# Optimization experiments

Hardware: AMD Instinct MI355X
Metric: run time of the kernel (lower is better)

The kernel has to match this reference:

```python
import jax, jax.numpy as jnp
import numpy as np

HIDDEN = 2048
N_HEADS = 16
N_KV = 4
HEAD_DIM = HIDDEN // N_HEADS  # 128


def setup_inputs() -> dict:
    key = jax.random.key(0)
    ks = jax.random.split(key, 9)
    s = 0.02
    kv_dim = N_KV * HEAD_DIM
    return {
        "x": jax.random.normal(ks[0], (2, 2048, HIDDEN), dtype=jnp.float32),
        "wq": jax.random.normal(ks[1], (HIDDEN, HIDDEN), dtype=jnp.float32) * s,
        "bq": jnp.zeros((HIDDEN,), jnp.float32),
        "wk": jax.random.normal(ks[2], (HIDDEN, kv_dim), dtype=jnp.float32) * s,
        "bk": jnp.zeros((kv_dim,), jnp.float32),
        "wv": jax.random.normal(ks[3], (HIDDEN, kv_dim), dtype=jnp.float32) * s,
        "bv": jnp.zeros((kv_dim,), jnp.float32),
        "wo": jax.random.normal(ks[4], (HIDDEN, HIDDEN), dtype=jnp.float32) * s,
        "bo": jnpp if False else jnp.zeros((HIDDEN,), jnp.float32),
    }


def reference(x, wq, bq, wk, bk, wv, bv, wo, bo):
    b, s, _ = x.shape
    rep = N_HEADS // N_KV
    # projections -> [b, heads, s, d]
    q = (x @ wq + bq).reshape(b, s, N_HEADS, HEAD_DIM).transpose(0, 2, 1, 3)
    k = (x @ wk + bk).reshape(b, s, N_KV, HEAD_DIM).transpose(0, 2, 1, 3)
    v = (x @ wv + bv).reshape(b, s, N_KV, HEAD_DIM).transpose(0, 2, 1, 3)
    # repeat_interleave KV heads to match Q heads
    k = jnp.repeat(k, rep, axis=1)
    v = jnp.repeat(v, rep, axis=1)
    scores = jnp.einsum("bhqd,bhkd->bhqk", q, k) / jnp.sqrt(jnp.float32(HEAD_DIM))
    attn = jax.nn.softmax(scores, axis=-1)  # dropout: eval mode (identity)
    out = jnp.einsum("bhqk,bhkd->bhqd", attn, v)
    out = out.transpose(0, 2, 1, 3).reshape(b, s, HIDDEN)
    return out @ wo + bo
```

## Files before the change

kernel.cpp:

```cpp
#include <hip/hip_runtime.h>

typedef short bf16x8 __attribute__((ext_vector_type(8)));
typedef float f32x4 __attribute__((ext_vector_type(4)));

__device__ __forceinline__ unsigned short f2b(float f) {
  union { float f; unsigned int u; } c; c.f = f;
  unsigned int u = c.u + 0x7fffu + ((c.u >> 16) & 1u);
  return (unsigned short)(u >> 16);
}

__device__ __forceinline__ void ld_g2l16(const void* g, void* l) {
  __builtin_amdgcn_global_load_lds(
      (__attribute__((address_space(1))) void*)(void*)g,
      (__attribute__((address_space(3))) void*)l, 16, 0, 0);
}


__global__ __launch_bounds__(256) void k_cvt(const float* __restrict__ in,
                                             unsigned short* __restrict__ out, int n) {
  int i = (blockIdx.x * 256 + threadIdx.x) * 4;
  const int stride = gridDim.x * 256 * 4;
  for (; i < n; i += stride) {
    const float4 v = *(const float4*)(in + i);
    unsigned short o0 = f2b(v.x), o1 = f2b(v.y), o2 = f2b(v.z), o3 = f2b(v.w);
    ushort4 o; o.x = o0; o.y = o1; o.z = o2; o.w = o3;
    *(ushort4*)(out + i) = o;
  }
}

__global__ __launch_bounds__(256) void k_tw(const float* __restrict__ W,
                                            unsigned short* __restrict__ Wt, int K, int N) {
  __shared__ float tile[32][33];
  const int nb = blockIdx.x * 32, kb = blockIdx.y * 32;
  const int tx = threadIdx.x & 31, ty = threadIdx.x >> 5;
#pragma unroll
  for (int i = 0; i < 32; i += 8)
    tile[ty + i][tx] = W[(size_t)(kb + ty + i) * N + nb + tx];
  __syncthreads();
#pragma unroll
  for (int i = 0; i < 32; i += 8)
    Wt[(size_t)(nb + ty + i) * K + kb + tx] = f2b(tile[tx][ty + i]);
}

__global__ __launch_bounds__(256) void k_tv(const unsigned short* __restrict__ v,
                                            unsigned short* __restrict__ vT) {
  __shared__ unsigned short tile[32][33];
  const int sb = blockIdx.x * 32, db = blockIdx.y * 32;
  const int ob = blockIdx.z, b = ob >> 2, kvh = ob & 3;
  const int tx = threadIdx.x & 31, ty = threadIdx.x >> 5;
#pragma unroll
  for (int i = 0; i < 32; i += 8)
    tile[ty + i][tx] = v[(size_t)(b * 2048 + sb + ty + i) * 1024 + 512 + kvh * 128 + db + tx];
  __syncthreads();
#pragma unroll
  for (int i = 0; i < 32; i += 8)
    vT[(size_t)ob * 262144 + (size_t)(db + ty + i) * 2048 + sb + tx] = tile[tx][ty + i];
}


template <int OUT_F32>
__global__ __launch_bounds__(256) void gemm_bt(const unsigned short* __restrict__ A,
                                               const unsigned short* __restrict__ Bt,
                                               const float* __restrict__ bias,
                                               const float* __restrict__ bias2,
                                               int nsplit,
                                               void* __restrict__ Cout,
                                               int M, int N, int K) {
  __shared__ unsigned short As[8192] __attribute__((aligned(16)));
  __shared__ unsigned short Bs[8192] __attribute__((aligned(16)));
  const int t = threadIdx.x, w = t >> 6, lane = t & 63;
  const int wr = w >> 1, wc = w & 1;
  const int bm = blockIdx.y, bn = blockIdx.x;

  f32x4 acc[4][4] = {};

  const int srow = w * 8 + (lane >> 3);
  const int scol = ((lane & 7) ^ (lane >> 3)) << 3;
  const unsigned short* Ap = A + (size_t)(bm * 128 + srow) * K + scol;
  const unsigned short* Bp = Bt + (size_t)(bn * 128 + srow) * K + scol;
  unsigned short* Ad = &As[(w * 64 + lane) * 8];
  unsigned short* Bd = &Bs[(w * 64 + lane) * 8];

  const int nkt = K >> 6;
  for (int kt = 0; kt < nkt; ++kt) {
#pragma unroll
    for (int i = 0; i < 4; ++i) {
      ld_g2l16(Ap + (size_t)i * 32 * K, Ad + i * 2048);
      ld_g2l16(Bp + (size_t)i * 32 * K, Bd + i * 2048);
    }
    Ap += 64; Bp += 64;
    __syncthreads();
#pragma unroll
    for (int kk = 0; kk < 2; ++kk) {
      bf16x8 av[4], bv[4];
#pragma unroll
      for (int m = 0; m < 4; ++m) {
        int r = wr * 64 + m * 16 + (lane & 15);
        int c = ((kk << 2) + (lane >> 4)) ^ (r & 7);
        av[m] = *(const bf16x8*)&As[r * 64 + c * 8];
      }
#pragma unroll
      for (int n = 0; n < 4; ++n) {
        int r = wc * 64 + n * 16 + (lane & 15);
        int c = ((kk << 2) + (lane >> 4)) ^ (r & 7);
        bv[n] = *(const bf16x8*)&Bs[r * 64 + c * 8];
      }
#pragma unroll
      for (int m = 0; m < 4; ++m)
#pragma unroll
        for (int n = 0; n < 4; ++n)
          acc[m][n] = __builtin_amdgcn_mfma_f32_16x16x32_bf16(av[m], bv[n], acc[m][n], 0, 0, 0);
    }
    __syncthreads();
  }

  const int row0 = bm * 128 + wr * 64 + ((lane >> 4) << 2);
  const int col0 = bn * 128 + wc * 64 + (lane & 15);
#pragma unroll
  for (int n = 0; n < 4; ++n) {
    const int c = col0 + n * 16;
    const float bb = (c < nsplit) ? bias[c] : bias2[c - nsplit];
#pragma unroll
    for (int m = 0; m < 4; ++m) {
#pragma unroll
      for (int j = 0; j < 4; ++j) {
        const float v = acc[m][n][j] + bb;
        const size_t idx = (size_t)(row0 + m * 16 + j) * N + c;
        if (OUT_F32) ((float*)Cout)[idx] = v;
        else ((unsigned short*)Cout)[idx] = f2b(v);
      }
    }
  }
}


__global__ __launch_bounds__(256, 4) void flash_gqa(const unsigned short* __restrict__ Q,
                                                    const unsigned short* __restrict__ Kx,
                                                    const unsigned short* __restrict__ Vt,
                                                    unsigned short* __restrict__ Oa) {
  __shared__ unsigned short smem[20480] __attribute__((aligned(16)));
  unsigned short* const Qs = smem;
  unsigned short* const Ks = smem;
  unsigned short* const Vs = smem + 8192;
  unsigned short* const Ps = smem + 16384;

  const int t = threadIdx.x, w = t >> 6, lane = t & 63;
  const int qt = blockIdx.x, bh = blockIdx.y;
  const int b = bh >> 4, h = bh & 15, kvh = h >> 2;

  const unsigned short* Qg = Q + (size_t)(b * 2048 + qt * 64) * 2048 + h * 128;
  const unsigned short* Kg = Kx + (size_t)(b * 2048) * 1024 + kvh * 128;
  const unsigned short* Vg = Vt + (size_t)(b * 4 + kvh) * 262144;

  {
    const int sc = ((t & 15) ^ ((t >> 4) & 7)) << 3;
    const unsigned short* src = Qg + (size_t)(t >> 4) * 2048 + sc;
    unsigned short* dst = &Qs[t * 8];
#pragma unroll
    for (int i = 0; i < 4; ++i) ld_g2l16(src + (size_t)i * 16 * 2048, dst + i * 2048);
  }
  __syncthreads();
  bf16x8 qf[4];
  {
    const int qr = w * 16 + (lane & 15);
#pragma unroll
    for (int kk = 0; kk < 4; ++kk) {
      const int c = ((kk << 2) + (lane >> 4)) ^ (qr & 7);
      qf[kk] = *(const bf16x8*)&Qs[qr * 128 + c * 8];
    }
  }
  __syncthreads();

  const float SC2 = 0.1275174246f;
  float m_run[4], l_run[4];
#pragma unroll
  for (int j = 0; j < 4; ++j) { m_run[j] = -1e30f; l_run[j] = 0.f; }
  f32x4 oacc[8] = {};

  const int ksc = ((t & 15) ^ ((t >> 4) & 7)) << 3;
  const int vsc = ((t & 7) ^ ((t >> 3) & 7)) << 3;
  unsigned short* const Kd = &Ks[t * 8];
  unsigned short* const Vd = &Vs[t * 8];

  for (int kt = 0; kt < 32; ++kt) {
    const unsigned short* ks = Kg + (size_t)(kt * 64 + (t >> 4)) * 1024 + ksc;
    const unsigned short* vs = Vg + (size_t)(t >> 3) * 2048 + kt * 64 + vsc;
#pragma unroll
    for (int i = 0; i < 4; ++i) {
      ld_g2l16(ks + (size_t)i * 16 * 1024, Kd + i * 2048);
      ld_g2l16(vs + (size_t)i * 32 * 2048, Vd + i * 2048);
    }
    __syncthreads();

    f32x4 sac[4] = {};
#pragma unroll
    for (int kk = 0; kk < 4; ++kk) {
      bf16x8 kf[4];
#pragma unroll
      for (int n = 0; n < 4; ++n) {
        const int r = n * 16 + (lane & 15);
        const int c = ((kk << 2) + (lane >> 4)) ^ (r & 7);
        kf[n] = *(const bf16x8*)&Ks[r * 128 + c * 8];
      }
#pragma unroll
      for (int n = 0; n < 4; ++n)
        sac[n] = __builtin_amdgcn_mfma_f32_16x16x32_bf16(qf[kk], kf[n], sac[n], 0, 0, 0);
    }

#pragma unroll
    for (int n = 0; n < 4; ++n)
#pragma unroll
      for (int j = 0; j < 4; ++j) sac[n][j] *= SC2;
#pragma unroll
    for (int j = 0; j < 4; ++j) {
      float tm = fmaxf(fmaxf(sac[0][j], sac[1][j]), fmaxf(sac[2][j], sac[3][j]));
#pragma unroll
      for (int off = 1; off < 16; off <<= 1) tm = fmaxf(tm, __shfl_xor(tm, off, 64));
      const float mn = fmaxf(m_run[j], tm);
      const float corr = exp2f(m_run[j] - mn);
      m_run[j] = mn;
      float rs = 0.f;
#pragma unroll
      for (int n = 0; n < 4; ++n) {
        const float p = exp2f(sac[n][j] - mn);
        sac[n][j] = p;
        rs += p;
      }
#pragma unroll
      for (int off = 1; off < 16; off <<= 1) rs += __shfl_xor(rs, off, 64);
      l_run[j] = l_run[j] * corr + rs;
#pragma unroll
      for (int di = 0; di < 8; ++di) oacc[di][j] *= corr;
    }

    {
      const int rbase = w * 16 + ((lane >> 4) << 2);
#pragma unroll
      for (int j = 0; j < 4; ++j) {
        const int r = rbase + j;
#pragma unroll
        for (int n = 0; n < 4; ++n) {
          const int col = n * 16 + (lane & 15);
          Ps[r * 64 + (((col >> 3) ^ (r & 7)) << 3) + (lane & 7)] = f2b(sac[n][j]);
        }
      }
    }

#pragma unroll
    for (int kk = 0; kk < 2; ++kk) {
      const int pr = w * 16 + (lane & 15);
      const int pc = ((kk << 2) + (lane >> 4)) ^ (pr & 7);
      const bf16x8 pf = *(const bf16x8*)&Ps[pr * 64 + pc * 8];
#pragma unroll
      for (int di = 0; di < 8; ++di) {
        const int r = di * 16 + (lane & 15);
        const int c = ((kk << 2) + (lane >> 4)) ^ (r & 7);
        const bf16x8 vf = *(const bf16x8*)&Vs[r * 64 + c * 8];
        oacc[di] = __builtin_amdgcn_mfma_f32_16x16x32_bf16(pf, vf, oacc[di], 0, 0, 0);
      }
    }
    __syncthreads();
  }

  {
    const int rbase = b * 2048 + qt * 64 + w * 16 + ((lane >> 4) << 2);
#pragma unroll
    for (int j = 0; j < 4; ++j) {
      const float inv = 1.0f / l_run[j];
#pragma unroll
      for (int di = 0; di < 8; ++di) {
        const int col = h * 128 + di * 16 + (lane & 15);
        Oa[(size_t)(rbase + j) * 2048 + col] = f2b(oacc[di][j] * inv);
      }
    }
  }
}


extern "C" void kernel_launch(void* const* d_in, const int* in_sizes, int n_in,
                              void* d_out, int out_size, void* d_ws, size_t ws_size,
                              hipStream_t stream) {
  (void)in_sizes; (void)n_in; (void)out_size; (void)ws_size;
  const float* x  = (const float*)d_in[0];
  const float* wq = (const float*)d_in[1];
  const float* bq = (const float*)d_in[2];
  const float* wk = (const float*)d_in[3];
  const float* bk = (const float*)d_in[4];
  const float* wv = (const float*)d_in[5];
  const float* bv = (const float*)d_in[6];
  const float* wo = (const float*)d_in[7];
  const float* bo = (const float*)d_in[8];

  char* ws = (char*)d_ws;
  unsigned short* xb  = (unsigned short*)(ws);
  unsigned short* qb  = (unsigned short*)(ws + 16777216);
  unsigned short* kvb = (unsigned short*)(ws + 33554432);
  unsigned short* vT  = (unsigned short*)(ws + 41943040);
  unsigned short* wqT = (unsigned short*)(ws + 46137344);
  unsigned short* wkT = (unsigned short*)(ws + 54525952);
  unsigned short* woT = (unsigned short*)(ws + 58720256);
  unsigned short* wvT = (unsigned short*)(ws + 56623104);

  k_cvt<<<4096, 256, 0, stream>>>(x, xb, 4096 * 2048);
  k_tw<<<dim3(64, 64), 256, 0, stream>>>(wq, wqT, 2048, 2048);
  k_tw<<<dim3(16, 64), 256, 0, stream>>>(wk, wkT, 2048, 512);
  k_tw<<<dim3(16, 64), 256, 0, stream>>>(wv, wvT, 2048, 512);
  k_tw<<<dim3(64, 64), 256, 0, stream>>>(wo, woT, 2048, 2048);

  gemm_bt<0><<<dim3(16, 32), 256, 0, stream>>>(xb, wqT, bq, bq, 1 << 30, qb, 4096, 2048, 2048);
  gemm_bt<0><<<dim3(8, 32), 256, 0, stream>>>(xb, wkT, bk, bv, 512, kvb, 4096, 1024, 2048);

  k_tv<<<dim3(64, 4, 8), 256, 0, stream>>>(kvb, vT);

  unsigned short* ao = xb;
  flash_gqa<<<dim3(32, 32), 256, 0, stream>>>(qb, kvb, vT, ao);

  gemm_bt<1><<<dim3(16, 32), 256, 0, stream>>>(ao, woT, bo, bo, 1 << 30, (float*)d_out, 4096, 2048, 2048);
}
```

Baseline: 425.8 us.

## Rewrite flash attention with 32x32 MFMA, transposed S, double-buffered K/V

The attention kernel now processes 128 query rows per block, with each wave owning 32 rows, and uses 32x32x16 MFMAs computing S^T so that P stays in registers (cvt_pk plus permlane32 swap) instead of going through shared memory. K/V tiles are double-buffered so the next tile's global-to-LDS load overlaps with compute. The online softmax rescale is skipped unless the max grows by more than a threshold, and the output is staged through LDS for coalesced 16-byte stores. This adds register pressure and doubles LDS use (occupancy hint drops to 2) and halves the grid.

```diff
diff --git a/kernel.cpp b/kernel.cpp
--- a/kernel.cpp
+++ b/kernel.cpp
@@ -2,11 +2,23 @@
 
 typedef short bf16x8 __attribute__((ext_vector_type(8)));
 typedef float f32x4 __attribute__((ext_vector_type(4)));
+typedef float f32x16 __attribute__((ext_vector_type(16)));
+typedef unsigned int u32;
 
 __device__ __forceinline__ unsigned short f2b(float f) {
   union { float f; unsigned int u; } c; c.f = f;
   unsigned int u = c.u + 0x7fffu + ((c.u >> 16) & 1u);
   return (unsigned short)(u >> 16);
+}
+
+__device__ __forceinline__ u32 cvtpk(float a, float b) {
+  u32 r;
+  asm("v_cvt_pk_bf16_f32 %0, %1, %2" : "=v"(r) : "v"(a), "v"(b));
+  return r;
+}
+
+__device__ __forceinline__ void pswap(u32& a, u32& b) {
+  asm("v_permlane32_swap_b32 %0, %1" : "+v"(a), "+v"(b));
 }
 
 __device__ __forceinline__ void ld_g2l16(const void* g, void* l) {
@@ -134,144 +146,185 @@
 }
 
 
-__global__ __launch_bounds__(256, 4) void flash_gqa(const unsigned short* __restrict__ Q,
+__global__ __launch_bounds__(256, 2) void flash_gqa(const unsigned short* __restrict__ Q,
                                                     const unsigned short* __restrict__ Kx,
                                                     const unsigned short* __restrict__ Vt,
                                                     unsigned short* __restrict__ Oa) {
-  __shared__ unsigned short smem[20480] __attribute__((aligned(16)));
-  unsigned short* const Qs = smem;
-  unsigned short* const Ks = smem;
-  unsigned short* const Vs = smem + 8192;
-  unsigned short* const Ps = smem + 16384;
-
+  __shared__ unsigned short smem[32768] __attribute__((aligned(16)));
   const int t = threadIdx.x, w = t >> 6, lane = t & 63;
+  const int lo = lane & 31, hi1 = lane >> 5;
   const int qt = blockIdx.x, bh = blockIdx.y;
   const int b = bh >> 4, h = bh & 15, kvh = h >> 2;
 
-  const unsigned short* Qg = Q + (size_t)(b * 2048 + qt * 64) * 2048 + h * 128;
+  const unsigned short* Qg = Q + (size_t)(b * 2048 + qt * 128) * 2048 + h * 128;
   const unsigned short* Kg = Kx + (size_t)(b * 2048) * 1024 + kvh * 128;
   const unsigned short* Vg = Vt + (size_t)(b * 4 + kvh) * 262144;
 
   {
     const int sc = ((t & 15) ^ ((t >> 4) & 7)) << 3;
     const unsigned short* src = Qg + (size_t)(t >> 4) * 2048 + sc;
-    unsigned short* dst = &Qs[t * 8];
-#pragma unroll
-    for (int i = 0; i < 4; ++i) ld_g2l16(src + (size_t)i * 16 * 2048, dst + i * 2048);
-  }
-  __syncthreads();
-  bf16x8 qf[4];
+    unsigned short* dst = &smem[t * 8];
+#pragma unroll
+    for (int i = 0; i < 8; ++i) ld_g2l16(src + (size_t)i * 16 * 2048, dst + i * 2048);
+  }
+  __syncthreads();
+  bf16x8 qf[8];
   {
-    const int qr = w * 16 + (lane & 15);
-#pragma unroll
-    for (int kk = 0; kk < 4; ++kk) {
-      const int c = ((kk << 2) + (lane >> 4)) ^ (qr & 7);
-      qf[kk] = *(const bf16x8*)&Qs[qr * 128 + c * 8];
-    }
-  }
-  __syncthreads();
+    const int r = w * 32 + lo;
+#pragma unroll
+    for (int kk = 0; kk < 8; ++kk) {
+      const int c8 = (2 * kk + hi1) ^ (r & 7);
+      qf[kk] = *(const bf16x8*)&smem[r * 128 + c8 * 8];
+    }
+  }
+  __syncthreads();
+
+  unsigned short* const K0 = smem;
+  unsigned short* const V0 = smem + 8192;
+  unsigned short* const K1 = smem + 16384;
+  unsigned short* const V1 = smem + 24576;
+
+  const int kchunk_src = ((t & 15) ^ ((t >> 4) & 7)) << 3;
+  const int vchunk_src = ((t & 7) ^ ((t >> 3) & 7)) << 3;
+
+  auto stage = [&](int kt, unsigned short* Kd, unsigned short* Vd) {
+    const unsigned short* ks = Kg + (size_t)(kt * 64 + (t >> 4)) * 1024 + kchunk_src;
+    const unsigned short* vs = Vg + (size_t)(t >> 3) * 2048 + kt * 64 + vchunk_src;
+#pragma unroll
+    for (int i = 0; i < 4; ++i) {
+      ld_g2l16(ks + (size_t)i * 16384, Kd + t * 8 + i * 2048);
+      ld_g2l16(vs + (size_t)i * 65536, Vd + t * 8 + i * 2048);
+    }
+  };
 
   const float SC2 = 0.1275174246f;
-  float m_run[4], l_run[4];
-#pragma unroll
-  for (int j = 0; j < 4; ++j) { m_run[j] = -1e30f; l_run[j] = 0.f; }
-  f32x4 oacc[8] = {};
-
-  const int ksc = ((t & 15) ^ ((t >> 4) & 7)) << 3;
-  const int vsc = ((t & 7) ^ ((t >> 3) & 7)) << 3;
-  unsigned short* const Kd = &Ks[t * 8];
-  unsigned short* const Vd = &Vs[t * 8];
+  float m_run = -1e30f, l_run = 0.f;
+  f32x16 oT[4] = {};
+
+  stage(0, K0, V0);
+  __syncthreads();
 
   for (int kt = 0; kt < 32; ++kt) {
-    const unsigned short* ks = Kg + (size_t)(kt * 64 + (t >> 4)) * 1024 + ksc;
-    const unsigned short* vs = Vg + (size_t)(t >> 3) * 2048 + kt * 64 + vsc;
+    unsigned short* const Kc = (kt & 1) ? K1 : K0;
+    unsigned short* const Vc = (kt & 1) ? V1 : V0;
+    if (kt < 31) stage(kt + 1, (kt & 1) ? K0 : K1, (kt & 1) ? V0 : V1);
+
+    f32x16 sa0 = {}, sa1 = {};
+    __builtin_amdgcn_s_setprio(1);
+#pragma unroll
+    for (int kk = 0; kk < 8; ++kk) {
+      const int c8 = (2 * kk + hi1) ^ (lo & 7);
+      const bf16x8 kf0 = *(const bf16x8*)&Kc[lo * 128 + c8 * 8];
+      const bf16x8 kf1 = *(const bf16x8*)&Kc[(32 + lo) * 128 + c8 * 8];
+      sa0 = __builtin_amdgcn_mfma_f32_32x32x16_bf16(kf0, qf[kk], sa0, 0, 0, 0);
+      sa1 = __builtin_amdgcn_mfma_f32_32x32x16_bf16(kf1, qf[kk], sa1, 0, 0, 0);
+    }
+    __builtin_amdgcn_s_setprio(0);
+
+    float tmax[8];
+#pragma unroll
+    for (int i = 0; i < 8; ++i) tmax[i] = fmaxf(sa0[i], sa0[i + 8]);
+#pragma unroll
+    for (int i = 0; i < 8; ++i) tmax[i] = fmaxf(tmax[i], fmaxf(sa1[i], sa1[i + 8]));
+    float tm = fmaxf(fmaxf(fmaxf(tmax[0], tmax[1]), fmaxf(tmax[2], tmax[3])),
+                     fmaxf(fmaxf(tmax[4], tmax[5]), fmaxf(tmax[6], tmax[7])));
+    tm *= SC2;
+    tm = fmaxf(tm, __shfl_xor(tm, 32, 64));
+
+    if (!__all(tm <= m_run + 8.f)) {
+      const float mn = fmaxf(m_run, tm);
+      const float corr = exp2f(m_run - mn);
+      m_run = mn;
+      l_run *= corr;
+#pragma unroll
+      for (int d = 0; d < 4; ++d)
+#pragma unroll
+        for (int i = 0; i < 16; ++i) oT[d][i] *= corr;
+    }
+
+    float r0 = 0.f, r1 = 0.f, r2 = 0.f, r3 = 0.f;
 #pragma unroll
     for (int i = 0; i < 4; ++i) {
-      ld_g2l16(ks + (size_t)i * 16 * 1024, Kd + i * 2048);
-      ld_g2l16(vs + (size_t)i * 32 * 2048, Vd + i * 2048);
-    }
+      float p0 = exp2f(fmaf(sa0[i], SC2, -m_run));      sa0[i] = p0;      r0 += p0;
+      float p1 = exp2f(fmaf(sa0[i + 4], SC2, -m_run));  sa0[i + 4] = p1;  r1 += p1;
+      float p2 = exp2f(fmaf(sa0[i + 8], SC2, -m_run));  sa0[i + 8] = p2;  r2 += p2;
+      float p3 = exp2f(fmaf(sa0[i + 12], SC2, -m_run)); sa0[i + 12] = p3; r3 += p3;
+    }
+#pragma unroll
+    for (int i = 0; i < 4; ++i) {
+      float p0 = exp2f(fmaf(sa1[i], SC2, -m_run));      sa1[i] = p0;      r0 += p0;
+      float p1 = exp2f(fmaf(sa1[i + 4], SC2, -m_run));  sa1[i + 4] = p1;  r1 += p1;
+      float p2 = exp2f(fmaf(sa1[i + 8], SC2, -m_run));  sa1[i + 8] = p2;  r2 += p2;
+      float p3 = exp2f(fmaf(sa1[i + 12], SC2, -m_run)); sa1[i + 12] = p3; r3 += p3;
+    }
+    float rs = (r0 + r1) + (r2 + r3);
+    rs += __shfl_xor(rs, 32, 64);
+    l_run += rs;
+
+    bf16x8 pf[4];
+#pragma unroll
+    for (int m = 0; m < 4; ++m) {
+      const int base = (m & 1) * 8;
+      u32 alo, ahi, blo, bhi;
+      if (m < 2) {
+        alo = cvtpk(sa0[base + 0], sa0[base + 1]);
+        ahi = cvtpk(sa0[base + 2], sa0[base + 3]);
+        blo = cvtpk(sa0[base + 4], sa0[base + 5]);
+        bhi = cvtpk(sa0[base + 6], sa0[base + 7]);
+      } else {
+        alo = cvtpk(sa1[base + 0], sa1[base + 1]);
+        ahi = cvtpk(sa1[base + 2], sa1[base + 3]);
+        blo = cvtpk(sa1[base + 4], sa1[base + 5]);
+        bhi = cvtpk(sa1[base + 6], sa1[base + 7]);
+      }
+      pswap(alo, blo);
+      pswap(ahi, bhi);
+      union { u32 u[4]; bf16x8 v; } pk;
+      pk.u[0] = alo; pk.u[1] = ahi; pk.u[2] = blo; pk.u[3] = bhi;
+      pf[m] = pk.v;
+    }
+
+    __builtin_amdgcn_s_setprio(1);
+#pragma unroll
+    for (int m = 0; m < 4; ++m) {
+#pragma unroll
+      for (int d = 0; d < 4; ++d) {
+        const int r = d * 32 + lo;
+        const int c = (2 * m + hi1) ^ (lo & 7);
+        const bf16x8 vf = *(const bf16x8*)&Vc[r * 64 + c * 8];
+        oT[d] = __builtin_amdgcn_mfma_f32_32x32x16_bf16(vf, pf[m], oT[d], 0, 0, 0);
+      }
+    }
+    __builtin_amdgcn_s_setprio(0);
     __syncthreads();
-
-    f32x4 sac[4] = {};
-#pragma unroll
-    for (int kk = 0; kk < 4; ++kk) {
-      bf16x8 kf[4];
-#pragma unroll
-      for (int n = 0; n < 4; ++n) {
-        const int r = n * 16 + (lane & 15);
-        const int c = ((kk << 2) + (lane >> 4)) ^ (r & 7);
-        kf[n] = *(const bf16x8*)&Ks[r * 128 + c * 8];
-      }
-#pragma unroll
-      for (int n = 0; n < 4; ++n)
-        sac[n] = __builtin_amdgcn_mfma_f32_16x16x32_bf16(qf[kk], kf[n], sac[n], 0, 0, 0);
-    }
-
-#pragma unroll
-    for (int n = 0; n < 4; ++n)
-#pragma unroll
-      for (int j = 0; j < 4; ++j) sac[n][j] *= SC2;
-#pragma unroll
-    for (int j = 0; j < 4; ++j) {
-      float tm = fmaxf(fmaxf(sac[0][j], sac[1][j]), fmaxf(sac[2][j], sac[3][j]));
-#pragma unroll
-      for (int off = 1; off < 16; off <<= 1) tm = fmaxf(tm, __shfl_xor(tm, off, 64));
-      const float mn = fmaxf(m_run[j], tm);
-      const float corr = exp2f(m_run[j] - mn);
-      m_run[j] = mn;
-      float rs = 0.f;
-#pragma unroll
-      for (int n = 0; n < 4; ++n) {
-        const float p = exp2f(sac[n][j] - mn);
-        sac[n][j] = p;
-        rs += p;
-      }
-#pragma unroll
-      for (int off = 1; off < 16; off <<= 1) rs += __shfl_xor(rs, off, 64);
-      l_run[j] = l_run[j] * corr + rs;
-#pragma unroll
-      for (int di = 0; di < 8; ++di) oacc[di][j] *= corr;
-    }
-
-    {
-      const int rbase = w * 16 + ((lane >> 4) << 2);
-#pragma unroll
-      for (int j = 0; j < 4; ++j) {
-        const int r = rbase + j;
-#pragma unroll
-        for (int n = 0; n < 4; ++n) {
-          const int col = n * 16 + (lane & 15);
-          Ps[r * 64 + (((col >> 3) ^ (r & 7)) << 3) + (lane & 7)] = f2b(sac[n][j]);
+  }
+
+  const float inv = 1.0f / l_run;
+  u32* const Ot = (u32*)smem;
+  {
+    const int row = w * 32 + lo;
+#pragma unroll
+    for (int d = 0; d < 4; ++d) {
+#pragma unroll
+      for (int j2 = 0; j2 < 4; ++j2) {
+#pragma unroll
+        for (int p = 0; p < 2; ++p) {
+          const int rg = 4 * j2 + 2 * p;
+          const u32 pk = cvtpk(oT[d][rg] * inv, oT[d][rg + 1] * inv);
+          const int dw = d * 16 + 4 * j2 + 2 * hi1 + p;
+          Ot[row * 64 + (((dw >> 2) ^ (row & 15)) << 2) + (dw & 3)] = pk;
         }
       }
     }
-
-#pragma unroll
-    for (int kk = 0; kk < 2; ++kk) {
-      const int pr = w * 16 + (lane & 15);
-      const int pc = ((kk << 2) + (lane >> 4)) ^ (pr & 7);
-      const bf16x8 pf = *(const bf16x8*)&Ps[pr * 64 + pc * 8];
-#pragma unroll
-      for (int di = 0; di < 8; ++di) {
-        const int r = di * 16 + (lane & 15);
-        const int c = ((kk << 2) + (lane >> 4)) ^ (r & 7);
-        const bf16x8 vf = *(const bf16x8*)&Vs[r * 64 + c * 8];
-        oacc[di] = __builtin_amdgcn_mfma_f32_16x16x32_bf16(pf, vf, oacc[di], 0, 0, 0);
-      }
-    }
-    __syncthreads();
-  }
-
+  }
+  __syncthreads();
   {
-    const int rbase = b * 2048 + qt * 64 + w * 16 + ((lane >> 4) << 2);
-#pragma unroll
-    for (int j = 0; j < 4; ++j) {
-      const float inv = 1.0f / l_run[j];
-#pragma unroll
-      for (int di = 0; di < 8; ++di) {
-        const int col = h * 128 + di * 16 + (lane & 15);
-        Oa[(size_t)(rbase + j) * 2048 + col] = f2b(oacc[di][j] * inv);
-      }
+#pragma unroll
+    for (int i = 0; i < 8; ++i) {
+      const int row = i * 16 + (t >> 4);
+      const int c4 = (t & 15) ^ (row & 15);
+      const int4 val = *(const int4*)&Ot[row * 64 + c4 * 4];
+      *(int4*)&Oa[(size_t)(b * 2048 + qt * 128 + row) * 2048 + h * 128 + (t & 15) * 8] = val;
     }
   }
 }
@@ -298,8 +351,8 @@
   unsigned short* vT  = (unsigned short*)(ws + 41943040);
   unsigned short* wqT = (unsigned short*)(ws + 46137344);
   unsigned short* wkT = (unsigned short*)(ws + 54525952);
+  unsigned short* wvT = (unsigned short*)(ws + 56623104);
   unsigned short* woT = (unsigned short*)(ws + 58720256);
-  unsigned short* wvT = (unsigned short*)(ws + 56623104);
 
   k_cvt<<<4096, 256, 0, stream>>>(x, xb, 4096 * 2048);
   k_tw<<<dim3(64, 64), 256, 0, stream>>>(wq, wqT, 2048, 2048);
@@ -313,7 +366,7 @@
   k_tv<<<dim3(64, 4, 8), 256, 0, stream>>>(kvb, vT);
 
   unsigned short* ao = xb;
-  flash_gqa<<<dim3(32, 32), 256, 0, stream>>>(qb, kvb, vT, ao);
+  flash_gqa<<<dim3(16, 32), 256, 0, stream>>>(qb, kvb, vT, ao);
 
   gemm_bt<1><<<dim3(16, 32), 256, 0, stream>>>(ao, woT, bo, bo, 1 << 30, (float*)d_out, 4096, 2048, 2048);
 }
```

Result: faster. 349.2 us (-18.0%).
